# Kernel tuning notes

Hardware: AMD Instinct MI355X
Metric: run time of the kernel (lower is better)

The kernel has to match this reference:

```python
import jax, jax.numpy as jnp
import numpy as np
from jax import lax

VOCAB = 30000
EMB = 300       # word_embedding_size (hardcoded in module)
H = 512         # opt.rnn_size (hidden_layer_dim)
HH = H // 2     # BiLSTM per-direction hidden
B = 128         # graphs per batch
L = 128         # nodes per graph
N = B * L       # total nodes
S = 10          # sample_size_per_layer
LAYERS = 7      # sample_layer_size


def _lstm(x, Wih, Whh, bih, bhh, reverse):
    # x: (B, L, EMB); returns (B, L, HH). PyTorch gate order i,f,g,o.
    xp = jnp.einsum('bld,gd->blg', x, Wih) + bih + bhh  # (B, L, 4HH)

    def step(carry, xt):
        h, c = carry
        g = xt + h @ Whh.T
        i, f, gg, o = jnp.split(g, 4, axis=-1)
        c = jax.nn.sigmoid(f) * c + jax.nn.sigmoid(i) * jnp.tanh(gg)
        h = jax.nn.sigmoid(o) * jnp.tanh(c)
        return (h, c), h

    h0 = jnp.zeros((x.shape[0], HH), x.dtype)
    _, hs = lax.scan(step, (h0, h0), jnp.swapaxes(xp, 0, 1), reverse=reverse)
    return jnp.swapaxes(hs, 0, 1)


def _agg(self_v, neigh, nlen, W, b):
    # GraphSAGE MeanAggregator with concat=True: relu(Linear(cat[self, mean(neigh)]))
    means = neigh.sum(1) / nlen[:, None]            # (N, H)
    return jax.nn.relu(jnp.concatenate([self_v, means], 1) @ W.T + b)


def setup_inputs():
    key = jax.random.key(0)
    ks = jax.random.split(key, 16)
    s = 0.05
    feature_info = jax.random.randint(ks[0], (N + 1, 1), 1, VOCAB, dtype=jnp.int32)
    batch_nodes = jnp.arange(N, dtype=jnp.int32).reshape(B, L)
    fw_adj_info = jax.random.randint(ks[1], (N + 1, S), 0, N + 1, dtype=jnp.int32)
    bw_adj_info = jax.random.randint(ks[2], (N + 1, S), 0, N + 1, dtype=jnp.int32)
    W_emb = (jax.random.normal(ks[3], (VOCAB, EMB)) * s).at[0].set(0.0)  # padding_idx=0
    Wih_f = jax.random.normal(ks[4], (4 * HH, EMB)) * s
    Whh_f = jax.random.normal(ks[5], (4 * HH, HH)) * s
    bih_f = jnp.zeros((4 * HH,)); bhh_f = jnp.zeros((4 * HH,))
    Wih_b = jax.random.normal(ks[6], (4 * HH, EMB)) * s
    Whh_b = jax.random.normal(ks[7], (4 * HH, HH)) * s
    bih_b = jnp.zeros((4 * HH,)); bhh_b = jnp.zeros((4 * HH,))
    padding_vec = jax.random.normal(ks[8], (1, H))
    fw_W = jax.random.normal(ks[9], (LAYERS, H, 2 * H)) * s
    fw_b = jnp.zeros((LAYERS, H))
    bw_W = jax.random.normal(ks[10], (LAYERS, H, 2 * H)) * s
    bw_b = jnp.zeros((LAYERS, H))
    return {
        'feature_info': feature_info, 'batch_nodes': batch_nodes,
        'fw_adj_info': fw_adj_info, 'bw_adj_info': bw_adj_info,
        'W_emb': W_emb, 'Wih_f': Wih_f, 'Whh_f': Whh_f, 'bih_f': bih_f, 'bhh_f': bhh_f,
        'Wih_b': Wih_b, 'Whh_b': Whh_b, 'bih_b': bih_b, 'bhh_b': bhh_b,
        'padding_vec': padding_vec, 'fw_W': fw_W, 'fw_b': fw_b, 'bw_W': bw_W, 'bw_b': bw_b,
    }


def reference(feature_info, batch_nodes, fw_adj_info, bw_adj_info, W_emb,
              Wih_f, Whh_f, bih_f, bhh_f, Wih_b, Whh_b, bih_b, bhh_b,
              padding_vec, fw_W, fw_b, bw_W, bw_b):
    Bn, Ln = batch_nodes.shape
    feat = feature_info[:-1, :].reshape(Bn, -1)              # (B, L)
    emb = W_emb[feat]                                        # (B, L, EMB)
    out_f = _lstm(emb, Wih_f, Whh_f, bih_f, bhh_f, False)
    out_b = _lstm(emb, Wih_b, Whh_b, bih_b, bhh_b, True)
    output_vector = jnp.concatenate([out_f, out_b], -1)      # (B, L, H)
    feature_vector = output_vector.reshape(-1, H)            # (N, H)
    node_repres = jnp.concatenate([feature_vector, padding_vec], 0)  # (N+1, H)
    nodes = batch_nodes.reshape(-1)
    fw_hidden = node_repres[nodes]
    bw_hidden = node_repres[nodes]
    # UniformNeighborSampler: gather adjacency rows, take S columns (deterministic sample)
    fw_nb = fw_adj_info[nodes][:, :S]
    bw_nb = bw_adj_info[nodes][:, :S]
    zero_row = jnp.zeros((1, H), fw_hidden.dtype)
    fw_len = bw_len = None
    for layer in range(LAYERS):
        li = min(layer, 6)
        if layer == 0:
            neigh = node_repres[fw_nb]                        # (N, S, H)
            fw_len = jnp.sign(jax.nn.relu(neigh).sum(2)).sum(1)
        else:
            neigh = jnp.concatenate([fw_hidden, zero_row], 0)[fw_nb]
        fw_hidden = _agg(fw_hidden, neigh, fw_len, fw_W[li], fw_b[li])
        if layer == 0:
            neighb = node_repres[bw_nb]
            bw_len = jnp.sign(jax.nn.relu(neighb).sum(2)).sum(1)
        else:
            neighb = jnp.concatenate([bw_hidden, zero_row], 0)[bw_nb]
        bw_hidden = _agg(bw_hidden, neighb, bw_len, bw_W[li], bw_b[li])
    hidden = jnp.concatenate([fw_hidden.reshape(-1, Ln, H),
                              bw_hidden.reshape(-1, Ln, H)], 2)   # (B, L, 2H)
    pooled = hidden.max(1)                                   # (B, 2H)
    graph_embedding = pooled.reshape(-1, H)                  # (2B, H)
    return hidden, graph_embedding, output_vector
```

## Files before the change

kernel.cpp:

```cpp
#include <hip/hip_runtime.h>
#include <hip/hip_bf16.h>
#include <math.h>

#define VOCABSZ 30000
#define EMB 300
#define HDIM 512
#define HH 256
#define G4 1024
#define BB 128
#define LL 128
#define NN 16384
#define SS 10
#define NLAYERS 7

typedef _Float16 f16;
typedef _Float16 half8 __attribute__((ext_vector_type(8)));
typedef float floatx4 __attribute__((ext_vector_type(4)));

#define OFF_XPF    0ll
#define OFF_XPB    16777216ll
#define WSB_WHH16  134217728ll
#define OFF_BSUM_F 34078720ll
#define OFF_BSUM_B 34079744ll
#define OFF_LENF   34080768ll
#define OFF_LENB   34097152ll
#define WSB_MEAN     0ll
#define WSB_H0       33554432ll
#define HBUF_HALVES  8389120ll
#define HBUF_BYTES   16778240ll
#define WSB_WF16     136454144ll
#define WF16_PER_DIR 3670016ll

#define HID_OFF 0ll
#define GE_OFF  16777216ll
#define OV_OFF  16908288ll

__device__ __forceinline__ float sigf(float x) { return 1.0f / (1.0f + expf(-x)); }

__global__ __launch_bounds__(256) void k_prep(const float* __restrict__ Whh_f,
                                              const float* __restrict__ Whh_b,
                                              const float* __restrict__ bih_f,
                                              const float* __restrict__ bhh_f,
                                              const float* __restrict__ bih_b,
                                              const float* __restrict__ bhh_b,
                                              float* __restrict__ ws,
                                              f16* __restrict__ whh16) {
    long i = (long)blockIdx.x * 256 + threadIdx.x;
    if (i < 262144) {
        whh16[i] = (f16)Whh_f[i];
    } else if (i < 524288) {
        whh16[i] = (f16)Whh_b[i - 262144];
    } else if (i < 525312) {
        int j = (int)(i - 524288);
        ws[OFF_BSUM_F + j] = bih_f[j] + bhh_f[j];
    } else if (i < 526336) {
        int j = (int)(i - 525312);
        ws[OFF_BSUM_B + j] = bih_b[j] + bhh_b[j];
    }
}

__global__ __launch_bounds__(256) void k_wconv(const float* __restrict__ fw_W,
                                               const float* __restrict__ bw_W,
                                               f16* __restrict__ dst) {
    const int b = blockIdx.x;
    const int dir = (b >= 3584);
    const float* __restrict__ src = dir ? bw_W : fw_W;
    f16* __restrict__ d = dst + (dir ? WF16_PER_DIR : 0);
    long e = (long)(dir ? b - 3584 : b) * 1024 + (long)threadIdx.x * 4;
    float4 v = *(const float4*)(src + e);
    f16 o[4] = {(f16)v.x, (f16)v.y, (f16)v.z, (f16)v.w};
    *(float2*)(d + e) = *(float2*)o;
}

__global__ __launch_bounds__(256) void k_xp(const int* __restrict__ feat,
                                            const float* __restrict__ W_emb,
                                            const float* __restrict__ Wih_f,
                                            const float* __restrict__ Wih_b,
                                            float* __restrict__ ws) {
    const int m0 = blockIdx.x * 64;
    const int j0 = blockIdx.y * 64;
    __shared__ float As[20][64];
    __shared__ float Bs[20][64];
    __shared__ int toks[64];
    const int tid = threadIdx.x;
    const int tx = tid & 15, ty = tid >> 4;
    if (tid < 64) toks[tid] = feat[m0 + tid];

    const int isF = (j0 < G4);
    const float* __restrict__ Wsrc = isF ? Wih_f : Wih_b;
    const int jb = isF ? j0 : j0 - G4;

    float acc[4][4] = {};
    for (int k0 = 0; k0 < 300; k0 += 20) {
        __syncthreads();
        for (int e = tid; e < 1280; e += 256) {
            int m = e / 20, k = e % 20;
            As[k][m] = W_emb[(long)toks[m] * EMB + k0 + k];
        }
        for (int e = tid; e < 1280; e += 256) {
            int j = e / 20, k = e % 20;
            Bs[k][j] = Wsrc[(long)(jb + j) * EMB + k0 + k];
        }
        __syncthreads();
#pragma unroll
        for (int k = 0; k < 20; ++k) {
            float a[4], b[4];
            *(float4*)a = *(const float4*)&As[k][ty * 4];
            *(float4*)b = *(const float4*)&Bs[k][tx * 4];
#pragma unroll
            for (int ii = 0; ii < 4; ++ii)
#pragma unroll
                for (int jj = 0; jj < 4; ++jj) acc[ii][jj] += a[ii] * b[jj];
        }
    }
    float* __restrict__ xp = ws + (isF ? OFF_XPF : OFF_XPB);
    const float* __restrict__ bs = ws + (isF ? OFF_BSUM_F : OFF_BSUM_B);
    float bv[4];
    *(float4*)bv = *(const float4*)&bs[jb + tx * 4];
#pragma unroll
    for (int ii = 0; ii < 4; ++ii) {
        long m = m0 + ty * 4 + ii;
        float4 o;
        o.x = acc[ii][0] + bv[0]; o.y = acc[ii][1] + bv[1];
        o.z = acc[ii][2] + bv[2]; o.w = acc[ii][3] + bv[3];
        *(float4*)&xp[m * G4 + jb + tx * 4] = o;
    }
}

__global__ __launch_bounds__(512) void k_lstm(const float* __restrict__ ws_ro,
                                              const f16* __restrict__ whh16,
                                              float* __restrict__ out) {
    const int dir = blockIdx.x >> 3;
    const int grp = blockIdx.x & 7;
    const int bid0 = grp * 16;
    const int tid = threadIdx.x;
    const int wv = tid >> 6, lane = tid & 63;
    const int n = lane & 15, kg = lane >> 4;

    __shared__ __align__(16) f16 ldsB[128 * 512];
    __shared__ __align__(16) f16 hbuf[8 * 512];

    const f16* __restrict__ whh = whh16 + (long)dir * 262144;
    const float* __restrict__ xp = ws_ro + (dir ? OFF_XPB : OFF_XPF);
    float* __restrict__ ov = out + OV_OFF;

#pragma unroll
    for (int i = 0; i < 16; ++i) {
        const int fid = wv * 16 + i;
        const int t = fid >> 6, w = (fid >> 3) & 7, kk = fid & 7;
        const int j = 16 * w + 128 * t + n;
        half8 v = *(const half8*)(whh + (long)j * 256 + kk * 32 + kg * 8);
        *(half8*)&ldsB[fid * 512 + lane * 8] = v;
    }
    {   half8 z = {};
        *(half8*)&hbuf[tid * 8] = z;
    }
    float cst[8] = {};
    __syncthreads();

    for (int ts = 0; ts < 128; ++ts) {
        const int tstep = dir ? (127 - ts) : ts;

        float xpv[8][4];
#pragma unroll
        for (int t = 0; t < 8; ++t)
#pragma unroll
            for (int r = 0; r < 4; ++r)
                xpv[t][r] = xp[((long)(bid0 + kg * 4 + r) * 128 + tstep) * 1024
                               + 16 * wv + 128 * t + n];

        floatx4 acc[8] = {};
        half8 sB[2][6];
#pragma unroll
        for (int t = 2; t < 8; ++t)
            sB[0][t - 2] = *(const half8*)(whh + (long)(16 * wv + 128 * t + n) * 256 + kg * 8);
#pragma unroll
        for (int kk = 0; kk < 8; ++kk) {
            const int cur = kk & 1, nxt = cur ^ 1;
            if (kk < 7) {
#pragma unroll
                for (int t = 2; t < 8; ++t)
                    sB[nxt][t - 2] = *(const half8*)(whh + (long)(16 * wv + 128 * t + n) * 256
                                                     + (kk + 1) * 32 + kg * 8);
            }
            half8 a  = *(const half8*)&hbuf[kk * 512 + lane * 8];
            half8 b0 = *(const half8*)&ldsB[((0 << 6) | (wv << 3) | kk) * 512 + lane * 8];
            half8 b1 = *(const half8*)&ldsB[((1 << 6) | (wv << 3) | kk) * 512 + lane * 8];
            acc[0] = __builtin_amdgcn_mfma_f32_16x16x32_f16(a, b0, acc[0], 0, 0, 0);
            acc[1] = __builtin_amdgcn_mfma_f32_16x16x32_f16(a, b1, acc[1], 0, 0, 0);
#pragma unroll
            for (int t = 2; t < 8; ++t)
                acc[t] = __builtin_amdgcn_mfma_f32_16x16x32_f16(a, sB[cur][t - 2], acc[t], 0, 0, 0);
        }
        __syncthreads();

#pragma unroll
        for (int t0 = 0; t0 < 2; ++t0) {
            const int u = 128 * t0 + 16 * wv + n;
            const int kkw = u >> 5;
            const int lgrp = 16 * ((u >> 3) & 3);
            const int e = u & 7;
#pragma unroll
            for (int r = 0; r < 4; ++r) {
                float gi = acc[t0][r]     + xpv[t0][r];
                float gf = acc[t0 + 2][r] + xpv[t0 + 2][r];
                float gg = acc[t0 + 4][r] + xpv[t0 + 4][r];
                float go = acc[t0 + 6][r] + xpv[t0 + 6][r];
                float c = cst[t0 * 4 + r];
                c = sigf(gf) * c + sigf(gi) * tanhf(gg);
                cst[t0 * 4 + r] = c;
                float h = sigf(go) * tanhf(c);
                hbuf[kkw * 512 + (kg * 4 + r + lgrp) * 8 + e] = (f16)h;
                ov[((long)(bid0 + kg * 4 + r) * 128 + tstep) * 512 + dir * 256 + u] = h;
            }
        }
        __syncthreads();
    }
}

__global__ __launch_bounds__(256) void k_init(const int* __restrict__ nodes,
                                              const float* __restrict__ padding,
                                              const float* __restrict__ out_ro,
                                              f16* __restrict__ h0) {
    long i = (long)blockIdx.x * 256 + threadIdx.x;
    if (i >= (long)NN * 64 + 256) return;
    if (i >= (long)NN * 64) {
        int e = (int)(i - (long)NN * 64);
        int buf = e >> 6, c = (e & 63) * 8;
        half8 z = {};
        *(half8*)(h0 + (long)buf * HBUF_HALVES + (long)NN * HDIM + c) = z;
        return;
    }
    int ni = (int)(i >> 6), c = (int)(i & 63) * 8;
    int r = nodes[ni];
    const float* src = (r < NN) ? (out_ro + OV_OFF + (long)r * HDIM + c)
                                : (padding + c);
    float4 v0 = *(const float4*)src;
    float4 v1 = *(const float4*)(src + 4);
    half8 h;
    h[0] = (f16)v0.x; h[1] = (f16)v0.y; h[2] = (f16)v0.z; h[3] = (f16)v0.w;
    h[4] = (f16)v1.x; h[5] = (f16)v1.y; h[6] = (f16)v1.z; h[7] = (f16)v1.w;
    *(half8*)(h0 + (long)ni * HDIM + c) = h;
    *(half8*)(h0 + 2 * HBUF_HALVES + (long)ni * HDIM + c) = h;
}

__global__ __launch_bounds__(256) void k_mean(const int* __restrict__ adj,
                                              const int* __restrict__ nodes,
                                              const f16* __restrict__ src,
                                              const float* __restrict__ ov,
                                              const float* __restrict__ padding,
                                              f16* __restrict__ mean,
                                              float* __restrict__ len,
                                              int layer0) {
    const int w = threadIdx.x >> 6;
    const int lane = threadIdx.x & 63;
    const int i = blockIdx.x * 4 + w;
    const int p0 = lane * 8;
    const int node = nodes[i];
    float acc[8] = {};
    float cnt = 0.0f;
    for (int s = 0; s < SS; ++s) {
        const int r = adj[(long)node * SS + s];
        if (layer0) {
            const float* row = (r < NN) ? (ov + (long)r * HDIM) : padding;
            float4 v0 = *(const float4*)(row + p0);
            float4 v1 = *(const float4*)(row + p0 + 4);
            acc[0] += v0.x; acc[1] += v0.y; acc[2] += v0.z; acc[3] += v0.w;
            acc[4] += v1.x; acc[5] += v1.y; acc[6] += v1.z; acc[7] += v1.w;
            float rs = fmaxf(v0.x, 0.f) + fmaxf(v0.y, 0.f) + fmaxf(v0.z, 0.f) + fmaxf(v0.w, 0.f)
                     + fmaxf(v1.x, 0.f) + fmaxf(v1.y, 0.f) + fmaxf(v1.z, 0.f) + fmaxf(v1.w, 0.f);
#pragma unroll
            for (int off = 32; off; off >>= 1) rs += __shfl_xor(rs, off);
            cnt += (rs > 0.0f) ? 1.0f : 0.0f;
        } else {
            half8 v = *(const half8*)(src + (long)r * HDIM + p0);
#pragma unroll
            for (int j = 0; j < 8; ++j) acc[j] += (float)v[j];
        }
    }
    float ln;
    if (layer0) {
        if (lane == 0) len[i] = cnt;
        ln = cnt;
    } else {
        ln = len[i];
    }
    half8 o;
#pragma unroll
    for (int j = 0; j < 8; ++j) o[j] = (f16)(acc[j] / ln);
    *(half8*)(mean + (long)i * HDIM + p0) = o;
}

__global__ __launch_bounds__(256) void k_sage(const f16* __restrict__ selfH,
                                              const f16* __restrict__ meanH,
                                              const f16* __restrict__ WH,
                                              const float* __restrict__ bl,
                                              f16* __restrict__ outH) {
    const int m0 = blockIdx.x * 128;
    const int q0 = blockIdx.y * 64;
    __shared__ __align__(16) f16 At[128 * 72];
    __shared__ __align__(16) f16 Bt[64 * 72];
    const int tid = threadIdx.x;
    const int wid = tid >> 6;
    const int lane = tid & 63;
    const int wr = wid >> 1, wc = wid & 1;
    const int ln15 = lane & 15, hi = lane >> 4;
    const int ar = tid >> 1, ac = (tid & 1) * 32;
    const int br = tid >> 2, bc = (tid & 3) * 16;

    floatx4 acc[4][2] = {};
    float4 av0, av1, av2, av3, bv0, bv1;

    {
        const f16* as = selfH + ((long)(m0 + ar) << 9) + ac;
        av0 = *(const float4*)(const void*)as;
        av1 = *(const float4*)(const void*)(as + 8);
        av2 = *(const float4*)(const void*)(as + 16);
        av3 = *(const float4*)(const void*)(as + 24);
        const f16* bs = WH + ((long)(q0 + br) << 10) + bc;
        bv0 = *(const float4*)(const void*)bs;
        bv1 = *(const float4*)(const void*)(bs + 8);
    }

    for (int k0 = 0; k0 < 1024; k0 += 64) {
        __syncthreads();
        *(float4*)(void*)&At[ar * 72 + ac]      = av0;
        *(float4*)(void*)&At[ar * 72 + ac + 8]  = av1;
        *(float4*)(void*)&At[ar * 72 + ac + 16] = av2;
        *(float4*)(void*)&At[ar * 72 + ac + 24] = av3;
        *(float4*)(void*)&Bt[br * 72 + bc]      = bv0;
        *(float4*)(void*)&Bt[br * 72 + bc + 8]  = bv1;
        __syncthreads();

        if (k0 + 64 < 1024) {
            const int kn = k0 + 64;
            const f16* as = (kn < 512)
                ? selfH + ((long)(m0 + ar) << 9) + kn + ac
                : meanH + ((long)(m0 + ar) << 9) + (kn - 512) + ac;
            av0 = *(const float4*)(const void*)as;
            av1 = *(const float4*)(const void*)(as + 8);
            av2 = *(const float4*)(const void*)(as + 16);
            av3 = *(const float4*)(const void*)(as + 24);
            const f16* bs = WH + ((long)(q0 + br) << 10) + kn + bc;
            bv0 = *(const float4*)(const void*)bs;
            bv1 = *(const float4*)(const void*)(bs + 8);
        }

#pragma unroll
        for (int ks = 0; ks < 2; ++ks) {
            half8 a[4], b[2];
#pragma unroll
            for (int mi = 0; mi < 4; ++mi)
                a[mi] = *(const half8*)(const void*)&At[(wr * 64 + mi * 16 + ln15) * 72 + ks * 32 + hi * 8];
#pragma unroll
            for (int ni = 0; ni < 2; ++ni)
                b[ni] = *(const half8*)(const void*)&Bt[(wc * 32 + ni * 16 + ln15) * 72 + ks * 32 + hi * 8];
#pragma unroll
            for (int mi = 0; mi < 4; ++mi)
#pragma unroll
                for (int ni = 0; ni < 2; ++ni)
                    acc[mi][ni] = __builtin_amdgcn_mfma_f32_16x16x32_f16(a[mi], b[ni], acc[mi][ni], 0, 0, 0);
        }
    }

#pragma unroll
    for (int ni = 0; ni < 2; ++ni) {
        const int gc = q0 + wc * 32 + ni * 16 + ln15;
        const float bv = bl[gc];
#pragma unroll
        for (int mi = 0; mi < 4; ++mi) {
            const int gr = m0 + wr * 64 + mi * 16 + hi * 4;
#pragma unroll
            for (int r = 0; r < 4; ++r) {
                float v = acc[mi][ni][r] + bv;
                v = fmaxf(v, 0.0f);
                outH[(long)(gr + r) * HDIM + gc] = (f16)v;
            }
        }
    }
}

__global__ __launch_bounds__(256) void k_final(const f16* __restrict__ fwF,
                                               const f16* __restrict__ bwF,
                                               float* __restrict__ out) {
    const int b = blockIdx.x >> 2;
    const int j = (blockIdx.x & 3) * 256 + threadIdx.x;
    const f16* __restrict__ src = (j < HDIM) ? fwF : bwF;
    const int jj = (j < HDIM) ? j : j - HDIM;
    float mx = -INFINITY;
    float* __restrict__ hid = out + HID_OFF;
#pragma unroll 4
    for (int l = 0; l < LL; ++l) {
        float v = (float)src[(long)(b * LL + l) * HDIM + jj];
        hid[(long)b * LL * 1024 + (long)l * 1024 + j] = v;
        mx = fmaxf(mx, v);
    }
    out[GE_OFF + (long)b * 1024 + j] = mx;
}

extern "C" void kernel_launch(void* const* d_in, const int* in_sizes, int n_in,
                              void* d_out, int out_size, void* d_ws, size_t ws_size,
                              hipStream_t stream) {
    const int*   feature_info = (const int*)d_in[0];
    const int*   batch_nodes  = (const int*)d_in[1];
    const int*   fw_adj       = (const int*)d_in[2];
    const int*   bw_adj       = (const int*)d_in[3];
    const float* W_emb        = (const float*)d_in[4];
    const float* Wih_f        = (const float*)d_in[5];
    const float* Whh_f        = (const float*)d_in[6];
    const float* bih_f        = (const float*)d_in[7];
    const float* bhh_f        = (const float*)d_in[8];
    const float* Wih_b        = (const float*)d_in[9];
    const float* Whh_b        = (const float*)d_in[10];
    const float* bih_b        = (const float*)d_in[11];
    const float* bhh_b        = (const float*)d_in[12];
    const float* padding      = (const float*)d_in[13];
    const float* fw_W         = (const float*)d_in[14];
    const float* fw_bias      = (const float*)d_in[15];
    const float* bw_W         = (const float*)d_in[16];
    const float* bw_bias      = (const float*)d_in[17];
    float* out = (float*)d_out;
    float* ws  = (float*)d_ws;
    char*  wsb = (char*)d_ws;

    f16* h0    = (f16*)(wsb + WSB_H0);
    f16* wf16  = (f16*)(wsb + WSB_WF16);
    f16* meanH = (f16*)(wsb + WSB_MEAN);
    f16* whh16 = (f16*)(wsb + WSB_WHH16);
    f16* fwH[2] = { h0,                    h0 + HBUF_HALVES };
    f16* bwH[2] = { h0 + 2 * HBUF_HALVES,  h0 + 3 * HBUF_HALVES };

    k_prep<<<2056, 256, 0, stream>>>(Whh_f, Whh_b, bih_f, bhh_f, bih_b, bhh_b, ws, whh16);
    k_wconv<<<7168, 256, 0, stream>>>(fw_W, bw_W, wf16);
    k_xp<<<dim3(256, 32), 256, 0, stream>>>(feature_info, W_emb, Wih_f, Wih_b, ws);
    k_lstm<<<16, 512, 0, stream>>>(ws, whh16, out);
    k_init<<<4097, 256, 0, stream>>>(batch_nodes, padding, out, h0);

    int fc = 0, bc = 0;
    for (int l = 0; l < NLAYERS; ++l) {
        k_mean<<<4096, 256, 0, stream>>>(fw_adj, batch_nodes, fwH[fc], out + OV_OFF,
                                         padding, meanH, ws + OFF_LENF, l == 0);
        k_sage<<<dim3(128, 8), 256, 0, stream>>>(fwH[fc], meanH,
                                                 wf16 + (long)l * HDIM * G4,
                                                 fw_bias + (long)l * HDIM, fwH[fc ^ 1]);
        fc ^= 1;
        k_mean<<<4096, 256, 0, stream>>>(bw_adj, batch_nodes, bwH[bc], out + OV_OFF,
                                         padding, meanH, ws + OFF_LENB, l == 0);
        k_sage<<<dim3(128, 8), 256, 0, stream>>>(bwH[bc], meanH,
                                                 wf16 + WF16_PER_DIR + (long)l * HDIM * G4,
                                                 bw_bias + (long)l * HDIM, bwH[bc ^ 1]);
        bc ^= 1;
    }
    k_final<<<512, 256, 0, stream>>>(fwH[fc], bwH[bc], out);
}
```

Baseline: 2.308 ms.

## Double-buffer LSTM hidden state, prefetch next step's inputs, widen SAGE GEMM tile

The LSTM recurrence kernel now double-buffers the hidden-state LDS buffer, which removes one barrier per timestep. It also prefetches the next step's xp projections and the first two streamed Whh k-slices before the gate math, and rotates a three-slot register pipeline for the streamed weights. The SAGE GEMM tile grows from 128x64 to 128x128 output, halving the grid and increasing A-operand reuse. In exchange, register pressure rises in both kernels, which may lower occupancy or cause spills, and the SAGE kernel launches fewer blocks.

```diff
diff --git a/kernel.cpp b/kernel.cpp
--- a/kernel.cpp
+++ b/kernel.cpp
@@ -127,9 +127,9 @@
     }
 }
 
-__global__ __launch_bounds__(512) void k_lstm(const float* __restrict__ ws_ro,
-                                              const f16* __restrict__ whh16,
-                                              float* __restrict__ out) {
+__global__ __launch_bounds__(512, 2) void k_lstm(const float* __restrict__ ws_ro,
+                                                 const f16* __restrict__ whh16,
+                                                 float* __restrict__ out) {
     const int dir = blockIdx.x >> 3;
     const int grp = blockIdx.x & 7;
     const int bid0 = grp * 16;
@@ -138,61 +138,82 @@
     const int n = lane & 15, kg = lane >> 4;
 
     __shared__ __align__(16) f16 ldsB[128 * 512];
-    __shared__ __align__(16) f16 hbuf[8 * 512];
+    __shared__ __align__(16) f16 hbuf[2][8 * 512];
 
     const f16* __restrict__ whh = whh16 + (long)dir * 262144;
     const float* __restrict__ xp = ws_ro + (dir ? OFF_XPB : OFF_XPF);
     float* __restrict__ ov = out + OV_OFF;
+
+    const f16* wbase[6];
+#pragma unroll
+    for (int t = 2; t < 8; ++t)
+        wbase[t - 2] = whh + (long)(16 * wv + 128 * t + n) * 256 + kg * 8;
 
 #pragma unroll
     for (int i = 0; i < 16; ++i) {
         const int fid = wv * 16 + i;
         const int t = fid >> 6, w = (fid >> 3) & 7, kk = fid & 7;
         const int j = 16 * w + 128 * t + n;
-        half8 v = *(const half8*)(whh + (long)j * 256 + kk * 32 + kg * 8);
-        *(half8*)&ldsB[fid * 512 + lane * 8] = v;
-    }
-    {   half8 z = {};
-        *(half8*)&hbuf[tid * 8] = z;
-    }
+        *(half8*)&ldsB[fid * 512 + lane * 8] =
+            *(const half8*)(whh + (long)j * 256 + kk * 32 + kg * 8);
+    }
+    { half8 z = {}; *(half8*)&hbuf[0][tid * 8] = z; }
+
     float cst[8] = {};
+    float xpv[8][4], xpn[8][4];
+    half8 sB[3][6];
+
+    {
+        const int t0s = dir ? 127 : 0;
+#pragma unroll
+        for (int t = 0; t < 6; ++t) sB[0][t] = *(const half8*)(wbase[t]);
+#pragma unroll
+        for (int t = 0; t < 6; ++t) sB[1][t] = *(const half8*)(wbase[t] + 32);
+#pragma unroll
+        for (int t = 0; t < 8; ++t)
+#pragma unroll
+            for (int r = 0; r < 4; ++r)
+                xpv[t][r] = xp[((long)(bid0 + kg * 4 + r) * 128 + t0s) * 1024
+                               + 16 * wv + 128 * t + n];
+    }
+    int p = 0;
     __syncthreads();
 
     for (int ts = 0; ts < 128; ++ts) {
         const int tstep = dir ? (127 - ts) : ts;
-
-        float xpv[8][4];
-#pragma unroll
-        for (int t = 0; t < 8; ++t)
-#pragma unroll
-            for (int r = 0; r < 4; ++r)
-                xpv[t][r] = xp[((long)(bid0 + kg * 4 + r) * 128 + tstep) * 1024
-                               + 16 * wv + 128 * t + n];
-
         floatx4 acc[8] = {};
-        half8 sB[2][6];
-#pragma unroll
-        for (int t = 2; t < 8; ++t)
-            sB[0][t - 2] = *(const half8*)(whh + (long)(16 * wv + 128 * t + n) * 256 + kg * 8);
 #pragma unroll
         for (int kk = 0; kk < 8; ++kk) {
-            const int cur = kk & 1, nxt = cur ^ 1;
-            if (kk < 7) {
-#pragma unroll
-                for (int t = 2; t < 8; ++t)
-                    sB[nxt][t - 2] = *(const half8*)(whh + (long)(16 * wv + 128 * t + n) * 256
-                                                     + (kk + 1) * 32 + kg * 8);
+            const int cur = kk % 3;
+            if (kk < 6) {
+                const int nslot = (kk + 2) % 3;
+#pragma unroll
+                for (int t = 0; t < 6; ++t)
+                    sB[nslot][t] = *(const half8*)(wbase[t] + (kk + 2) * 32);
             }
-            half8 a  = *(const half8*)&hbuf[kk * 512 + lane * 8];
-            half8 b0 = *(const half8*)&ldsB[((0 << 6) | (wv << 3) | kk) * 512 + lane * 8];
-            half8 b1 = *(const half8*)&ldsB[((1 << 6) | (wv << 3) | kk) * 512 + lane * 8];
+            half8 a  = *(const half8*)&hbuf[p][kk * 512 + lane * 8];
+            half8 b0 = *(const half8*)&ldsB[(((0 << 6) | (wv << 3) | kk)) * 512 + lane * 8];
+            half8 b1 = *(const half8*)&ldsB[(((1 << 6) | (wv << 3) | kk)) * 512 + lane * 8];
             acc[0] = __builtin_amdgcn_mfma_f32_16x16x32_f16(a, b0, acc[0], 0, 0, 0);
             acc[1] = __builtin_amdgcn_mfma_f32_16x16x32_f16(a, b1, acc[1], 0, 0, 0);
 #pragma unroll
             for (int t = 2; t < 8; ++t)
                 acc[t] = __builtin_amdgcn_mfma_f32_16x16x32_f16(a, sB[cur][t - 2], acc[t], 0, 0, 0);
         }
-        __syncthreads();
+
+        if (ts < 127) {
+            const int tnx = dir ? (127 - (ts + 1)) : (ts + 1);
+#pragma unroll
+            for (int t = 0; t < 6; ++t) sB[0][t] = *(const half8*)(wbase[t]);
+#pragma unroll
+            for (int t = 0; t < 6; ++t) sB[1][t] = *(const half8*)(wbase[t] + 32);
+#pragma unroll
+            for (int t = 0; t < 8; ++t)
+#pragma unroll
+                for (int r = 0; r < 4; ++r)
+                    xpn[t][r] = xp[((long)(bid0 + kg * 4 + r) * 128 + tnx) * 1024
+                                   + 16 * wv + 128 * t + n];
+        }
 
 #pragma unroll
         for (int t0 = 0; t0 < 2; ++t0) {
@@ -210,11 +231,16 @@
                 c = sigf(gf) * c + sigf(gi) * tanhf(gg);
                 cst[t0 * 4 + r] = c;
                 float h = sigf(go) * tanhf(c);
-                hbuf[kkw * 512 + (kg * 4 + r + lgrp) * 8 + e] = (f16)h;
+                hbuf[p ^ 1][kkw * 512 + (kg * 4 + r + lgrp) * 8 + e] = (f16)h;
                 ov[((long)(bid0 + kg * 4 + r) * 128 + tstep) * 512 + dir * 256 + u] = h;
             }
         }
         __syncthreads();
+#pragma unroll
+        for (int t = 0; t < 8; ++t)
+#pragma unroll
+            for (int r = 0; r < 4; ++r) xpv[t][r] = xpn[t][r];
+        p ^= 1;
     }
 }
 
@@ -297,75 +323,80 @@
                                               const float* __restrict__ bl,
                                               f16* __restrict__ outH) {
     const int m0 = blockIdx.x * 128;
-    const int q0 = blockIdx.y * 64;
+    const int q0 = blockIdx.y * 128;
     __shared__ __align__(16) f16 At[128 * 72];
-    __shared__ __align__(16) f16 Bt[64 * 72];
+    __shared__ __align__(16) f16 Bt[128 * 72];
     const int tid = threadIdx.x;
     const int wid = tid >> 6;
     const int lane = tid & 63;
     const int wr = wid >> 1, wc = wid & 1;
     const int ln15 = lane & 15, hi = lane >> 4;
-    const int ar = tid >> 1, ac = (tid & 1) * 32;
-    const int br = tid >> 2, bc = (tid & 3) * 16;
-
-    floatx4 acc[4][2] = {};
-    float4 av0, av1, av2, av3, bv0, bv1;
+    const int ar = tid >> 1, acS = (tid & 1) * 32;
+
+    floatx4 acc[4][4] = {};
+    float4 av0, av1, av2, av3, bv0, bv1, bv2, bv3;
 
     {
-        const f16* as = selfH + ((long)(m0 + ar) << 9) + ac;
+        const f16* as = selfH + ((long)(m0 + ar) << 9) + acS;
         av0 = *(const float4*)(const void*)as;
         av1 = *(const float4*)(const void*)(as + 8);
         av2 = *(const float4*)(const void*)(as + 16);
         av3 = *(const float4*)(const void*)(as + 24);
-        const f16* bs = WH + ((long)(q0 + br) << 10) + bc;
+        const f16* bs = WH + ((long)(q0 + ar) << 10) + acS;
         bv0 = *(const float4*)(const void*)bs;
         bv1 = *(const float4*)(const void*)(bs + 8);
+        bv2 = *(const float4*)(const void*)(bs + 16);
+        bv3 = *(const float4*)(const void*)(bs + 24);
     }
 
     for (int k0 = 0; k0 < 1024; k0 += 64) {
         __syncthreads();
-        *(float4*)(void*)&At[ar * 72 + ac]      = av0;
-        *(float4*)(void*)&At[ar * 72 + ac + 8]  = av1;
-        *(float4*)(void*)&At[ar * 72 + ac + 16] = av2;
-        *(float4*)(void*)&At[ar * 72 + ac + 24] = av3;
-        *(float4*)(void*)&Bt[br * 72 + bc]      = bv0;
-        *(float4*)(void*)&Bt[br * 72 + bc + 8]  = bv1;
+        *(float4*)(void*)&At[ar * 72 + acS]      = av0;
+        *(float4*)(void*)&At[ar * 72 + acS + 8]  = av1;
+        *(float4*)(void*)&At[ar * 72 + acS + 16] = av2;
+        *(float4*)(void*)&At[ar * 72 + acS + 24] = av3;
+        *(float4*)(void*)&Bt[ar * 72 + acS]      = bv0;
+        *(float4*)(void*)&Bt[ar * 72 + acS + 8]  = bv1;
+        *(float4*)(void*)&Bt[ar * 72 + acS + 16] = bv2;
+        *(float4*)(void*)&Bt[ar * 72 + acS + 24] = bv3;
         __syncthreads();
 
         if (k0 + 64 < 1024) {
             const int kn = k0 + 64;
             const f16* as = (kn < 512)
-                ? selfH + ((long)(m0 + ar) << 9) + kn + ac
-                : meanH + ((long)(m0 + ar) << 9) + (kn - 512) + ac;
+                ? selfH + ((long)(m0 + ar) << 9) + kn + acS
+                : meanH + ((long)(m0 + ar) << 9) + (kn - 512) + acS;
             av0 = *(const float4*)(const void*)as;
             av1 = *(const float4*)(const void*)(as + 8);
             av2 = *(const float4*)(const void*)(as + 16);
             av3 = *(const float4*)(const void*)(as + 24);
-            const f16* bs = WH + ((long)(q0 + br) << 10) + kn + bc;
+            const f16* bs = WH + ((long)(q0 + ar) << 10) + kn + acS;
             bv0 = *(const float4*)(const void*)bs;
             bv1 = *(const float4*)(const void*)(bs + 8);
+            bv2 = *(const float4*)(const void*)(bs + 16);
+            bv3 = *(const float4*)(const void*)(bs + 24);
         }
 
 #pragma unroll
         for (int ks = 0; ks < 2; ++ks) {
-            half8 a[4], b[2];
+            half8 a[4], b[4];
 #pragma unroll
             for (int mi = 0; mi < 4; ++mi)
                 a[mi] = *(const half8*)(const void*)&At[(wr * 64 + mi * 16 + ln15) * 72 + ks * 32 + hi * 8];
 #pragma unroll
-            for (int ni = 0; ni < 2; ++ni)
-                b[ni] = *(const half8*)(const void*)&Bt[(wc * 32 + ni * 16 + ln15) * 72 + ks * 32 + hi * 8];
+            for (int ni = 0; ni < 4; ++ni)
+                b[ni] = *(const half8*)(const void*)&Bt[(wc * 64 + ni * 16 + ln15) * 72 + ks * 32 + hi * 8];
 #pragma unroll
             for (int mi = 0; mi < 4; ++mi)
 #pragma unroll
-                for (int ni = 0; ni < 2; ++ni)
+                for (int ni = 0; ni < 4; ++ni)
                     acc[mi][ni] = __builtin_amdgcn_mfma_f32_16x16x32_f16(a[mi], b[ni], acc[mi][ni], 0, 0, 0);
         }
     }
 
 #pragma unroll
-    for (int ni = 0; ni < 2; ++ni) {
-        const int gc = q0 + wc * 32 + ni * 16 + ln15;
+    for (int ni = 0; ni < 4; ++ni) {
+        const int gc = q0 + wc * 64 + ni * 16 + ln15;
         const float bv = bl[gc];
 #pragma unroll
         for (int mi = 0; mi < 4; ++mi) {
@@ -440,13 +471,13 @@
     for (int l = 0; l < NLAYERS; ++l) {
         k_mean<<<4096, 256, 0, stream>>>(fw_adj, batch_nodes, fwH[fc], out + OV_OFF,
                                          padding, meanH, ws + OFF_LENF, l == 0);
-        k_sage<<<dim3(128, 8), 256, 0, stream>>>(fwH[fc], meanH,
+        k_sage<<<dim3(128, 4), 256, 0, stream>>>(fwH[fc], meanH,
                                                  wf16 + (long)l * HDIM * G4,
                                                  fw_bias + (long)l * HDIM, fwH[fc ^ 1]);
         fc ^= 1;
         k_mean<<<4096, 256, 0, stream>>>(bw_adj, batch_nodes, bwH[bc], out + OV_OFF,
                                          padding, meanH, ws + OFF_LENB, l == 0);
-        k_sage<<<dim3(128, 8), 256, 0, stream>>>(bwH[bc], meanH,
+        k_sage<<<dim3(128, 4), 256, 0, stream>>>(bwH[bc], meanH,
                                                  wf16 + WF16_PER_DIR + (long)l * HDIM * G4,
                                                  bw_bias + (long)l * HDIM, bwH[bc ^ 1]);
         bc ^= 1;
```

After: 2.501 ms. 1.08x slower.
